# Performance work log

Measured on AMD Instinct MI355X. Metric: run time of the kernel, lower is better.

The kernel has to match this reference:

```python
import jax, jax.numpy as jnp
import numpy as np
from jax import lax

SIGMA, GAMMA, N_ORI = 6.0, 0.5, 6
WAVELENGTHS = (8.0, 10.0, 12.0)
KS = 37  # int(6*sigma)=36 -> +1 to make odd


def make_gabor_kernels():
    # Replicates cv2.getGaborKernel(psi=0); kernel is symmetric under 180-deg
    # rotation so cv2's index flip is a no-op and conv == correlation.
    half = KS // 2
    yy, xx = np.meshgrid(np.arange(-half, half + 1, dtype=np.float64),
                         np.arange(-half, half + 1, dtype=np.float64), indexing='ij')
    ks = []
    for lam in WAVELENGTHS:
        for t in range(N_ORI):
            th = t * np.pi / N_ORI
            xr = xx * np.cos(th) + yy * np.sin(th)
            yr = -xx * np.sin(th) + yy * np.cos(th)
            k = np.exp(-(xr ** 2 + (GAMMA ** 2) * yr ** 2) / (2.0 * SIGMA ** 2)) \
                * np.cos(2.0 * np.pi / lam * xr)
            ks.append(k.astype(np.float32))
    return jnp.asarray(np.stack(ks))[:, None]  # (F=18, 1, 37, 37)


def setup_inputs() -> dict:
    key = jax.random.key(0)
    x = jax.random.normal(key, (8, 3, 256, 256), dtype=jnp.float32)
    return {"x": x, "gabor_kernels": make_gabor_kernels()}


def haar_dwt2(x):
    # Single-level pywt haar dwt2; for even H,W symmetric padding never fires,
    # so each output pixel comes from a disjoint 2x2 block [[a,b],[c,d]].
    B, C, H, W = x.shape
    xb = x.reshape(B, C, H // 2, 2, W // 2, 2)
    a, b = xb[:, :, :, 0, :, 0], xb[:, :, :, 0, :, 1]
    c, d = xb[:, :, :, 1, :, 0], xb[:, :, :, 1, :, 1]
    LL = (a + b + c + d) * 0.5
    LH = (a + b - c - d) * 0.5  # pywt cH ('da'): high along rows
    HL = (a - b + c - d) * 0.5  # pywt cV ('ad'): high along cols
    HH = (a - b - c + d) * 0.5  # pywt cD ('dd')
    sub = jnp.stack([LL, LH, HL, HH], axis=2)  # (B, C, 4, H/2, W/2)
    return sub.reshape(B, C * 4, H // 2, W // 2)


def gabor_bank(x, kernels):
    # One grouped conv replaces the Python C x F conv2d loop. Group-major output
    # channel order (channel outer, filter inner) matches the torch loop order.
    B, C, H, W = x.shape
    F = kernels.shape[0]
    w = jnp.tile(kernels, (C, 1, 1, 1))  # (C*F, 1, KS, KS)
    pad = KS // 2
    return lax.conv_general_dilated(
        x, w, window_strides=(1, 1), padding=[(pad, pad), (pad, pad)],
        dimension_numbers=('NCHW', 'OIHW', 'NCHW'), feature_group_count=C)


def fft_channels(x):
    B, C, H, W = x.shape
    xc = jnp.fft.rfft2(x, norm='ortho')       # (B, C, H, W//2+1)
    mag = jnp.abs(xc)
    ph = jnp.arctan2(xc.imag, xc.real)        # torch.angle
    pad = W - mag.shape[-1]
    pads = [(0, 0), (0, 0), (0, 0), (0, pad)]
    return jnp.concatenate([jnp.pad(mag, pads), jnp.pad(ph, pads)], axis=1)


def reference(x, gabor_kernels):
    dwt = haar_dwt2(x)                 # (B, C*4, H/2, W/2)
    gab = gabor_bank(x, gabor_kernels)  # (B, C*18, H, W)
    fft = fft_channels(x)              # (B, C*2, H, W)
    return (dwt, gab, fft)
```

## Files before the change

### kernel.cpp

```cpp
#include <hip/hip_runtime.h>
#include <math.h>

#define BB 8
#define CC 3
#define HH 256
#define WW 256
#define KSZ 37
#define PD 18

#define DWT_OFF 0
#define GAB_OFF (8*12*128*128)
#define FFT_OFF (GAB_OFF + 8*54*256*256)

#define PSTRIDE 88

typedef short bf16x8 __attribute__((ext_vector_type(8)));
typedef float f32x16 __attribute__((ext_vector_type(16)));

__device__ __forceinline__ unsigned f2bf(float f) {
  unsigned u = __float_as_uint(f);
  return (u + 0x7fffu + ((u >> 16) & 1u)) >> 16;
}

__global__ __launch_bounds__(256) void prep_wshc_kernel(
    const float* __restrict__ wk, ushort* __restrict__ wshc) {
  int idx = blockIdx.x * 256 + threadIdx.x;
  if (idx >= 454656) return;
  int j = idx & 7; int rest = idx >> 3;
  int l = rest & 63; rest >>= 6;
  int t = rest % 3; rest /= 3;
  int ky = rest % 37; int s = rest / 37;
  int m = l & 31, hi = l >> 5;
  int kk = 16 * t + 8 * hi + j - s;
  float v = 0.0f;
  if (m < 18 && kk >= 0 && kk < 37) v = wk[(m * 37 + ky) * 37 + kk];
  wshc[idx] = (ushort)f2bf(v);
}

#define LOAD_B_SET \
    r0 = *reinterpret_cast<const bf16x8*>(bp); \
    r1 = *reinterpret_cast<const bf16x8*>(bp + 8); \
    r2 = *reinterpret_cast<const bf16x8*>(bp + 16); \
    r3 = *reinterpret_cast<const bf16x8*>(bp + 24); \
    r4 = *reinterpret_cast<const bf16x8*>(bp + 32); \
    r5 = *reinterpret_cast<const bf16x8*>(bp + 40); \
    r6 = *reinterpret_cast<const bf16x8*>(bp + 48); \
    r7 = *reinterpret_cast<const bf16x8*>(bp + 56);
#define MFMA_GROUP(A0, A1, A2) \
    acc0 = __builtin_amdgcn_mfma_f32_32x32x16_bf16(A0, r0, acc0, 0, 0, 0); \
    acc1 = __builtin_amdgcn_mfma_f32_32x32x16_bf16(A0, r1, acc1, 0, 0, 0); \
    acc2 = __builtin_amdgcn_mfma_f32_32x32x16_bf16(A0, r2, acc2, 0, 0, 0); \
    acc3 = __builtin_amdgcn_mfma_f32_32x32x16_bf16(A0, r3, acc3, 0, 0, 0); \
    acc0 = __builtin_amdgcn_mfma_f32_32x32x16_bf16(A1, r2, acc0, 0, 0, 0); \
    acc1 = __builtin_amdgcn_mfma_f32_32x32x16_bf16(A1, r3, acc1, 0, 0, 0); \
    acc2 = __builtin_amdgcn_mfma_f32_32x32x16_bf16(A1, r4, acc2, 0, 0, 0); \
    acc3 = __builtin_amdgcn_mfma_f32_32x32x16_bf16(A1, r5, acc3, 0, 0, 0); \
    acc0 = __builtin_amdgcn_mfma_f32_32x32x16_bf16(A2, r4, acc0, 0, 0, 0); \
    acc1 = __builtin_amdgcn_mfma_f32_32x32x16_bf16(A2, r5, acc1, 0, 0, 0); \
    acc2 = __builtin_amdgcn_mfma_f32_32x32x16_bf16(A2, r6, acc2, 0, 0, 0); \
    acc3 = __builtin_amdgcn_mfma_f32_32x32x16_bf16(A2, r7, acc3, 0, 0, 0);

__global__ __launch_bounds__(512, 4) void gabor_mfma_kernel(
    const float* __restrict__ x, const ushort* __restrict__ wshc,
    float* __restrict__ out) {
  __shared__ unsigned patchU[68 * (PSTRIDE / 2)];
  __shared__ float cbuf[4 * 32 * 33];

  const int tid = threadIdx.x;
  const int tileX = (blockIdx.x & 7) * 32;
  const int tileY = (blockIdx.x >> 3) * 32;
  const int cin = blockIdx.y, b = blockIdx.z;
  const float* xp = x + (size_t)(b * CC + cin) * (HH * WW);

  for (int idx = tid; idx < 68 * (PSTRIDE / 2); idx += 512) {
    int r = idx / (PSTRIDE / 2), dc = idx - r * (PSTRIDE / 2);
    int gy = tileY + r - PD;
    int gx0 = tileX + 2 * dc - PD;
    float v0 = 0.0f, v1 = 0.0f;
    if ((unsigned)gy < 256u) {
      if ((unsigned)gx0 < 256u)       v0 = xp[gy * WW + gx0];
      if ((unsigned)(gx0 + 1) < 256u) v1 = xp[gy * WW + gx0 + 1];
    }
    patchU[idx] = f2bf(v0) | (f2bf(v1) << 16);
  }
  __syncthreads();

  const int w  = tid >> 6;
  const int l  = tid & 63;
  const int n  = l & 31;
  const int hi = l >> 5;

  f32x16 acc0 = {0.f,0.f,0.f,0.f,0.f,0.f,0.f,0.f,0.f,0.f,0.f,0.f,0.f,0.f,0.f,0.f};
  f32x16 acc1 = acc0, acc2 = acc0, acc3 = acc0;

  const ushort* patchS = reinterpret_cast<const ushort*>(patchU);
  const ushort* ap = wshc + (size_t)w * (37 * 3 * 512) + (size_t)l * 8;
  const ushort* bp = patchS + (size_t)n * PSTRIDE + hi * 8;

  bf16x8 aA0, aA1, aA2, aB0, aB1, aB2;
  bf16x8 r0, r1, r2, r3, r4, r5, r6, r7;

  aA0 = *reinterpret_cast<const bf16x8*>(ap);
  aA1 = *reinterpret_cast<const bf16x8*>(ap + 512);
  aA2 = *reinterpret_cast<const bf16x8*>(ap + 1024);

  for (int kp = 0; kp < 18; ++kp) {
    aB0 = *reinterpret_cast<const bf16x8*>(ap + 1536);
    aB1 = *reinterpret_cast<const bf16x8*>(ap + 2048);
    aB2 = *reinterpret_cast<const bf16x8*>(ap + 2560);
    LOAD_B_SET
    MFMA_GROUP(aA0, aA1, aA2)
    bp += PSTRIDE;
    aA0 = *reinterpret_cast<const bf16x8*>(ap + 3072);
    aA1 = *reinterpret_cast<const bf16x8*>(ap + 3584);
    aA2 = *reinterpret_cast<const bf16x8*>(ap + 4096);
    LOAD_B_SET
    MFMA_GROUP(aB0, aB1, aB2)
    ap += 3072;
    bp += PSTRIDE;
  }
  {
    LOAD_B_SET
    MFMA_GROUP(aA0, aA1, aA2)
  }
  __syncthreads();

  float* outb = out + GAB_OFF + (size_t)(b * 54 + cin * 18) * (HH * WW);
#pragma unroll
  for (int g = 0; g < 5; ++g) {
    if (hi == (g & 1)) {
      const int rq = g >> 1;
#pragma unroll
      for (int q = 0; q < 4; ++q) {
        const int e = 4 * rq + q;
        float* crow = &cbuf[(q * 32 + n) * 33 + w];
        crow[0]  = acc0[e];
        crow[8]  = acc1[e];
        crow[16] = acc2[e];
        crow[24] = acc3[e];
      }
    }
    __syncthreads();
#pragma unroll
    for (int it = 0; it < 8; ++it) {
      int idx = tid + it * 512;
      int xo = idx & 31, yo = (idx >> 5) & 31, q = idx >> 10;
      int f = 4 * g + q;
      if (f < 18)
        outb[(size_t)f * (HH * WW) + (size_t)(tileY + yo) * WW + tileX + xo] =
            cbuf[(q * 32 + yo) * 33 + xo];
    }
    __syncthreads();
  }
}

__global__ __launch_bounds__(256) void haar_dwt_kernel(
    const float* __restrict__ x, float* __restrict__ out) {
  int idx = blockIdx.x * 256 + threadIdx.x;
  if (idx >= BB * CC * 128 * 128) return;
  int j  = idx & 127;
  int i  = (idx >> 7) & 127;
  int bc = idx >> 14;
  const float* xp = x + (size_t)bc * (HH * WW);
  float2 top = *reinterpret_cast<const float2*>(&xp[(2 * i) * WW + 2 * j]);
  float2 bot = *reinterpret_cast<const float2*>(&xp[(2 * i + 1) * WW + 2 * j]);
  float a = top.x, b = top.y, c = bot.x, d = bot.y;
  int bI = bc / 3, cI = bc % 3;
  float* op = out + DWT_OFF + ((size_t)(bI * 12 + cI * 4) * 128 + i) * 128 + j;
  op[0]     = (a + b + c + d) * 0.5f;
  op[16384] = (a + b - c - d) * 0.5f;
  op[32768] = (a - b + c - d) * 0.5f;
  op[49152] = (a - b - c + d) * 0.5f;
}

__global__ __launch_bounds__(64) void fft_rows_kernel(
    const float* __restrict__ x, float* __restrict__ stg) {
  __shared__ float re[256], im[256], twr[128], twi[128];
  const int rowid = blockIdx.x;
  const float* xr = x + (size_t)rowid * 256;
  const int t = threadIdx.x;

#pragma unroll
  for (int q = 0; q < 2; ++q) {
    int k = t + q * 64;
    float sn, cs;
    sincosf(-2.0f * (float)M_PI * (float)k / 256.0f, &sn, &cs);
    twr[k] = cs; twi[k] = sn;
  }
#pragma unroll
  for (int q = 0; q < 4; ++q) {
    int i = t + q * 64;
    int br = __brev((unsigned)i) >> 24;
    re[br] = xr[i];
    im[br] = 0.0f;
  }
  __syncthreads();

  for (int s = 1; s <= 8; ++s) {
    int half = 1 << (s - 1);
    int sh = 8 - s;
#pragma unroll
    for (int q = 0; q < 2; ++q) {
      int j = t + q * 64;
      int g = j >> (s - 1);
      int p = j & (half - 1);
      int i1 = (g << s) + p;
      int i2 = i1 + half;
      float cs = twr[p << sh], sn = twi[p << sh];
      float r2 = re[i2], m2 = im[i2];
      float tr = r2 * cs - m2 * sn;
      float ti = r2 * sn + m2 * cs;
      float r1 = re[i1], m1 = im[i1];
      re[i2] = r1 - tr; im[i2] = m1 - ti;
      re[i1] = r1 + tr; im[i1] = m1 + ti;
    }
    __syncthreads();
  }

  float* sr = stg + (size_t)rowid * 258;
#pragma unroll
  for (int q = 0; q < 3; ++q) {
    int k = t + q * 64;
    if (k <= 128) {
      sr[2 * k]     = re[k];
      sr[2 * k + 1] = im[k];
    }
  }
}

__global__ __launch_bounds__(64) void fft_cols_kernel(
    const float* __restrict__ stg, float* __restrict__ outf) {
  const int k  = blockIdx.x & 255;
  const int bc = blockIdx.x >> 8;
  const int b  = bc / 3;
  const int c  = bc - b * 3;
  const int t  = threadIdx.x;
  float* magp = outf + (size_t)(b * 6 + c) * (HH * WW);
  float* php  = outf + (size_t)(b * 6 + c + 3) * (HH * WW);

  if (k >= 129) {
#pragma unroll
    for (int q = 0; q < 4; ++q) {
      int u = t + q * 64;
      magp[(size_t)u * WW + k] = 0.0f;
      php[(size_t)u * WW + k]  = 0.0f;
    }
    return;
  }

  __shared__ float re[256], im[256], twr[128], twi[128];
  const float* sp = stg + (size_t)bc * (256 * 258);
#pragma unroll
  for (int q = 0; q < 2; ++q) {
    int kk = t + q * 64;
    float sn, cs;
    sincosf(-2.0f * (float)M_PI * (float)kk / 256.0f, &sn, &cs);
    twr[kk] = cs; twi[kk] = sn;
  }
#pragma unroll
  for (int q = 0; q < 4; ++q) {
    int y = t + q * 64;
    int br = __brev((unsigned)y) >> 24;
    re[br] = sp[(size_t)y * 258 + 2 * k];
    im[br] = sp[(size_t)y * 258 + 2 * k + 1];
  }
  __syncthreads();

  for (int s = 1; s <= 8; ++s) {
    int half = 1 << (s - 1);
    int sh = 8 - s;
#pragma unroll
    for (int q = 0; q < 2; ++q) {
      int j = t + q * 64;
      int g = j >> (s - 1);
      int p = j & (half - 1);
      int i1 = (g << s) + p;
      int i2 = i1 + half;
      float cs = twr[p << sh], sn = twi[p << sh];
      float r2 = re[i2], m2 = im[i2];
      float tr = r2 * cs - m2 * sn;
      float ti = r2 * sn + m2 * cs;
      float r1 = re[i1], m1 = im[i1];
      re[i2] = r1 - tr; im[i2] = m1 - ti;
      re[i1] = r1 + tr; im[i1] = m1 + ti;
    }
    __syncthreads();
  }

  const float scale = 1.0f / 256.0f;
#pragma unroll
  for (int q = 0; q < 4; ++q) {
    int u = t + q * 64;
    float r = re[u], m = im[u];
    magp[(size_t)u * WW + k] = sqrtf(r * r + m * m) * scale;
    php[(size_t)u * WW + k]  = atan2f(m, r);
  }
}

extern "C" void kernel_launch(void* const* d_in, const int* in_sizes, int n_in,
                              void* d_out, int out_size, void* d_ws, size_t ws_size,
                              hipStream_t stream) {
  const float* x  = (const float*)d_in[0];
  const float* wk = (const float*)d_in[1];
  float* out = (float*)d_out;

  ushort* wshc = (ushort*)(out + DWT_OFF);
  float*  stg  = out + GAB_OFF;

  prep_wshc_kernel<<<dim3(1776), dim3(256), 0, stream>>>(wk, wshc);
  fft_rows_kernel<<<dim3(BB * CC * HH), dim3(64), 0, stream>>>(x, stg);
  fft_cols_kernel<<<dim3(BB * CC * WW), dim3(64), 0, stream>>>(stg, out + FFT_OFF);
  gabor_mfma_kernel<<<dim3(64, CC, BB), dim3(512), 0, stream>>>(x, wshc, out);
  haar_dwt_kernel<<<dim3(1536), dim3(256), 0, stream>>>(x, out);
}
```

Baseline: 189.9 us.

## Fuse weight prep with row FFT and Gabor conv with column FFT

Merges the weight-prep and row-FFT kernels into one launch, and the Gabor MFMA conv and column-FFT kernels into another, dispatching on block index. The FFTs are restructured so each 64-lane wave handles one row or column with no block barriers. This relies on in-order LDS access within a single wave. The intermediate spectrum is now staged in place in the FFT output region instead of the Gabor region, so the column FFT can share a launch with the Gabor conv. The goal is fewer launches and letting the light FFT blocks fill the device alongside the heavy conv blocks, at the cost of relying on implicit intra-wave LDS ordering.

```diff
diff --git a/kernel.cpp b/kernel.cpp
--- a/kernel.cpp
+++ b/kernel.cpp
@@ -14,6 +14,11 @@
 
 #define PSTRIDE 88
 
+#define PREP_BLOCKS 888
+#define FFTROW_BLOCKS 768
+#define GAB_BLOCKS 1536
+#define FFTCOL_BLOCKS 768
+
 typedef short bf16x8 __attribute__((ext_vector_type(8)));
 typedef float f32x16 __attribute__((ext_vector_type(16)));
 
@@ -22,19 +27,84 @@
   return (u + 0x7fffu + ((u >> 16) & 1u)) >> 16;
 }
 
-__global__ __launch_bounds__(256) void prep_wshc_kernel(
-    const float* __restrict__ wk, ushort* __restrict__ wshc) {
-  int idx = blockIdx.x * 256 + threadIdx.x;
-  if (idx >= 454656) return;
-  int j = idx & 7; int rest = idx >> 3;
-  int l = rest & 63; rest >>= 6;
-  int t = rest % 3; rest /= 3;
-  int ky = rest % 37; int s = rest / 37;
-  int m = l & 31, hi = l >> 5;
-  int kk = 16 * t + 8 * hi + j - s;
-  float v = 0.0f;
-  if (m < 18 && kk >= 0 && kk < 37) v = wk[(m * 37 + ky) * 37 + kk];
-  wshc[idx] = (ushort)f2bf(v);
+__global__ __launch_bounds__(512) void fused_pre_kernel(
+    const float* __restrict__ x, const float* __restrict__ wk,
+    ushort* __restrict__ wshc, float* __restrict__ out) {
+  __shared__ __align__(16) float smem[4352];
+  const int g = blockIdx.x;
+  const int tid = threadIdx.x;
+
+  if (g < PREP_BLOCKS) {
+    int idx = g * 512 + tid;
+    int j = idx & 7; int rest = idx >> 3;
+    int l = rest & 63; rest >>= 6;
+    int t = rest % 3; rest /= 3;
+    int ky = rest % 37; int s = rest / 37;
+    int m = l & 31, hi = l >> 5;
+    int kk = 16 * t + 8 * hi + j - s;
+    float v = 0.0f;
+    if (m < 18 && kk >= 0 && kk < 37) v = wk[(m * 37 + ky) * 37 + kk];
+    wshc[idx] = (ushort)f2bf(v);
+    return;
+  }
+
+  const int w = tid >> 6;
+  const int t = tid & 63;
+  const int rowid = (g - PREP_BLOCKS) * 8 + w;
+  float* re  = smem + w * 256;
+  float* im  = smem + 2048 + w * 256;
+  float* twr = smem + 4096;
+  float* twi = smem + 4224;
+
+#pragma unroll
+  for (int q = 0; q < 2; ++q) {
+    int k = t + q * 64;
+    float sn, cs;
+    sincosf(-2.0f * (float)M_PI * (float)k / 256.0f, &sn, &cs);
+    twr[k] = cs; twi[k] = sn;
+  }
+
+  const float* xr = x + (size_t)rowid * 256;
+#pragma unroll
+  for (int q = 0; q < 4; ++q) {
+    int i = t + q * 64;
+    int br = __brev((unsigned)i) >> 24;
+    re[br] = xr[i];
+    im[br] = 0.0f;
+  }
+
+  for (int s = 1; s <= 8; ++s) {
+    int half = 1 << (s - 1);
+    int sh = 8 - s;
+#pragma unroll
+    for (int q = 0; q < 2; ++q) {
+      int j = t + q * 64;
+      int gg = j >> (s - 1);
+      int p = j & (half - 1);
+      int i1 = (gg << s) + p;
+      int i2 = i1 + half;
+      float cs = twr[p << sh], sn = twi[p << sh];
+      float r2 = re[i2], m2 = im[i2];
+      float tr = r2 * cs - m2 * sn;
+      float ti = r2 * sn + m2 * cs;
+      float r1 = re[i1], m1 = im[i1];
+      re[i2] = r1 - tr; im[i2] = m1 - ti;
+      re[i1] = r1 + tr; im[i1] = m1 + ti;
+    }
+  }
+
+  const int bc = rowid >> 8;
+  const int y  = rowid & 255;
+  const int b  = bc / 3, c = bc - b * 3;
+  float* magrow = out + FFT_OFF + (size_t)(b * 6 + c) * (HH * WW) + (size_t)y * WW;
+  float* phrow  = magrow + (size_t)3 * (HH * WW);
+#pragma unroll
+  for (int q = 0; q < 2; ++q) {
+    int k = t + q * 64;
+    magrow[k] = re[k];
+    phrow[k]  = im[k];
+  }
+  if (t == 0) { magrow[128] = re[128]; phrow[128] = im[128]; }
 }
 
 #define LOAD_B_SET \
@@ -60,97 +130,163 @@
     acc2 = __builtin_amdgcn_mfma_f32_32x32x16_bf16(A2, r6, acc2, 0, 0, 0); \
     acc3 = __builtin_amdgcn_mfma_f32_32x32x16_bf16(A2, r7, acc3, 0, 0, 0);
 
-__global__ __launch_bounds__(512, 4) void gabor_mfma_kernel(
+__global__ __launch_bounds__(512, 4) void fused_main_kernel(
     const float* __restrict__ x, const ushort* __restrict__ wshc,
     float* __restrict__ out) {
-  __shared__ unsigned patchU[68 * (PSTRIDE / 2)];
-  __shared__ float cbuf[4 * 32 * 33];
-
+  __shared__ __align__(16) float smem[7216];
+  const int g = blockIdx.x;
   const int tid = threadIdx.x;
-  const int tileX = (blockIdx.x & 7) * 32;
-  const int tileY = (blockIdx.x >> 3) * 32;
-  const int cin = blockIdx.y, b = blockIdx.z;
-  const float* xp = x + (size_t)(b * CC + cin) * (HH * WW);
-
-  for (int idx = tid; idx < 68 * (PSTRIDE / 2); idx += 512) {
-    int r = idx / (PSTRIDE / 2), dc = idx - r * (PSTRIDE / 2);
-    int gy = tileY + r - PD;
-    int gx0 = tileX + 2 * dc - PD;
-    float v0 = 0.0f, v1 = 0.0f;
-    if ((unsigned)gy < 256u) {
-      if ((unsigned)gx0 < 256u)       v0 = xp[gy * WW + gx0];
-      if ((unsigned)(gx0 + 1) < 256u) v1 = xp[gy * WW + gx0 + 1];
-    }
-    patchU[idx] = f2bf(v0) | (f2bf(v1) << 16);
-  }
-  __syncthreads();
-
-  const int w  = tid >> 6;
-  const int l  = tid & 63;
-  const int n  = l & 31;
-  const int hi = l >> 5;
-
-  f32x16 acc0 = {0.f,0.f,0.f,0.f,0.f,0.f,0.f,0.f,0.f,0.f,0.f,0.f,0.f,0.f,0.f,0.f};
-  f32x16 acc1 = acc0, acc2 = acc0, acc3 = acc0;
-
-  const ushort* patchS = reinterpret_cast<const ushort*>(patchU);
-  const ushort* ap = wshc + (size_t)w * (37 * 3 * 512) + (size_t)l * 8;
-  const ushort* bp = patchS + (size_t)n * PSTRIDE + hi * 8;
-
-  bf16x8 aA0, aA1, aA2, aB0, aB1, aB2;
-  bf16x8 r0, r1, r2, r3, r4, r5, r6, r7;
-
-  aA0 = *reinterpret_cast<const bf16x8*>(ap);
-  aA1 = *reinterpret_cast<const bf16x8*>(ap + 512);
-  aA2 = *reinterpret_cast<const bf16x8*>(ap + 1024);
-
-  for (int kp = 0; kp < 18; ++kp) {
-    aB0 = *reinterpret_cast<const bf16x8*>(ap + 1536);
-    aB1 = *reinterpret_cast<const bf16x8*>(ap + 2048);
-    aB2 = *reinterpret_cast<const bf16x8*>(ap + 2560);
-    LOAD_B_SET
-    MFMA_GROUP(aA0, aA1, aA2)
-    bp += PSTRIDE;
-    aA0 = *reinterpret_cast<const bf16x8*>(ap + 3072);
-    aA1 = *reinterpret_cast<const bf16x8*>(ap + 3584);
-    aA2 = *reinterpret_cast<const bf16x8*>(ap + 4096);
-    LOAD_B_SET
-    MFMA_GROUP(aB0, aB1, aB2)
-    ap += 3072;
-    bp += PSTRIDE;
-  }
-  {
-    LOAD_B_SET
-    MFMA_GROUP(aA0, aA1, aA2)
-  }
-  __syncthreads();
-
-  float* outb = out + GAB_OFF + (size_t)(b * 54 + cin * 18) * (HH * WW);
-#pragma unroll
-  for (int g = 0; g < 5; ++g) {
-    if (hi == (g & 1)) {
-      const int rq = g >> 1;
-#pragma unroll
-      for (int q = 0; q < 4; ++q) {
-        const int e = 4 * rq + q;
-        float* crow = &cbuf[(q * 32 + n) * 33 + w];
-        crow[0]  = acc0[e];
-        crow[8]  = acc1[e];
-        crow[16] = acc2[e];
-        crow[24] = acc3[e];
+
+  if (g < GAB_BLOCKS) {
+    unsigned* patchU = reinterpret_cast<unsigned*>(smem);
+    float* cbuf = smem + 2992;
+    const int tile = g & 63;
+    const int rest = g >> 6;
+    const int cin = rest % 3, b = rest / 3;
+    const int tileX = (tile & 7) * 32;
+    const int tileY = (tile >> 3) * 32;
+    const float* xp = x + (size_t)(b * CC + cin) * (HH * WW);
+
+    for (int idx = tid; idx < 68 * (PSTRIDE / 2); idx += 512) {
+      int r = idx / (PSTRIDE / 2), dc = idx - r * (PSTRIDE / 2);
+      int gy = tileY + r - PD;
+      int gx0 = tileX + 2 * dc - PD;
+      float v0 = 0.0f, v1 = 0.0f;
+      if ((unsigned)gy < 256u) {
+        if ((unsigned)gx0 < 256u)       v0 = xp[gy * WW + gx0];
+        if ((unsigned)(gx0 + 1) < 256u) v1 = xp[gy * WW + gx0 + 1];
       }
+      patchU[idx] = f2bf(v0) | (f2bf(v1) << 16);
     }
     __syncthreads();
-#pragma unroll
-    for (int it = 0; it < 8; ++it) {
-      int idx = tid + it * 512;
-      int xo = idx & 31, yo = (idx >> 5) & 31, q = idx >> 10;
-      int f = 4 * g + q;
-      if (f < 18)
-        outb[(size_t)f * (HH * WW) + (size_t)(tileY + yo) * WW + tileX + xo] =
-            cbuf[(q * 32 + yo) * 33 + xo];
+
+    const int w  = tid >> 6;
+    const int l  = tid & 63;
+    const int n  = l & 31;
+    const int hi = l >> 5;
+
+    f32x16 acc0 = {0.f,0.f,0.f,0.f,0.f,0.f,0.f,0.f,0.f,0.f,0.f,0.f,0.f,0.f,0.f,0.f};
+    f32x16 acc1 = acc0, acc2 = acc0, acc3 = acc0;
+
+    const ushort* patchS = reinterpret_cast<const ushort*>(patchU);
+    const ushort* ap = wshc + (size_t)w * (37 * 3 * 512) + (size_t)l * 8;
+    const ushort* bp = patchS + (size_t)n * PSTRIDE + hi * 8;
+
+    bf16x8 aA0, aA1, aA2, aB0, aB1, aB2;
+    bf16x8 r0, r1, r2, r3, r4, r5, r6, r7;
+
+    aA0 = *reinterpret_cast<const bf16x8*>(ap);
+    aA1 = *reinterpret_cast<const bf16x8*>(ap + 512);
+    aA2 = *reinterpret_cast<const bf16x8*>(ap + 1024);
+
+    for (int kp = 0; kp < 18; ++kp) {
+      aB0 = *reinterpret_cast<const bf16x8*>(ap + 1536);
+      aB1 = *reinterpret_cast<const bf16x8*>(ap + 2048);
+      aB2 = *reinterpret_cast<const bf16x8*>(ap + 2560);
+      LOAD_B_SET
+      MFMA_GROUP(aA0, aA1, aA2)
+      bp += PSTRIDE;
+      aA0 = *reinterpret_cast<const bf16x8*>(ap + 3072);
+      aA1 = *reinterpret_cast<const bf16x8*>(ap + 3584);
+      aA2 = *reinterpret_cast<const bf16x8*>(ap + 4096);
+      LOAD_B_SET
+      MFMA_GROUP(aB0, aB1, aB2)
+      ap += 3072;
+      bp += PSTRIDE;
+    }
+    {
+      LOAD_B_SET
+      MFMA_GROUP(aA0, aA1, aA2)
     }
     __syncthreads();
+
+    float* outb = out + GAB_OFF + (size_t)(b * 54 + cin * 18) * (HH * WW);
+#pragma unroll
+    for (int gq = 0; gq < 5; ++gq) {
+      if (hi == (gq & 1)) {
+        const int rq = gq >> 1;
+#pragma unroll
+        for (int q = 0; q < 4; ++q) {
+          const int e = 4 * rq + q;
+          float* crow = &cbuf[(q * 32 + n) * 33 + w];
+          crow[0]  = acc0[e];
+          crow[8]  = acc1[e];
+          crow[16] = acc2[e];
+          crow[24] = acc3[e];
+        }
+      }
+      __syncthreads();
+#pragma unroll
+      for (int it = 0; it < 8; ++it) {
+        int idx = tid + it * 512;
+        int xo = idx & 31, yo = (idx >> 5) & 31, q = idx >> 10;
+        int f = 4 * gq + q;
+        if (f < 18)
+          outb[(size_t)f * (HH * WW) + (size_t)(tileY + yo) * WW + tileX + xo] =
+              cbuf[(q * 32 + yo) * 33 + xo];
+      }
+      __syncthreads();
+    }
+    return;
+  }
+
+  const int w = tid >> 6;
+  const int t = tid & 63;
+  const int colid = (g - GAB_BLOCKS) * 8 + w;
+  const int bc = colid >> 8;
+  const int k  = colid & 255;
+  const int b  = bc / 3, c = bc - b * 3;
+  float* re  = smem + w * 256;
+  float* im  = smem + 2048 + w * 256;
+  float* twr = smem + 4096;
+  float* twi = smem + 4224;
+
+#pragma unroll
+  for (int q = 0; q < 2; ++q) {
+    int kk = t + q * 64;
+    float sn, cs;
+    sincosf(-2.0f * (float)M_PI * (float)kk / 256.0f, &sn, &cs);
+    twr[kk] = cs; twi[kk] = sn;
+  }
+
+  float* magp = out + FFT_OFF + (size_t)(b * 6 + c) * (HH * WW);
+  float* php  = magp + (size_t)3 * (HH * WW);
+  const bool live = (k < 129);
+#pragma unroll
+  for (int q = 0; q < 4; ++q) {
+    int y = t + q * 64;
+    int br = __brev((unsigned)y) >> 24;
+    re[br] = live ? magp[(size_t)y * WW + k] : 0.0f;
+    im[br] = live ? php[(size_t)y * WW + k]  : 0.0f;
+  }
+
+  for (int s = 1; s <= 8; ++s) {
+    int half = 1 << (s - 1);
+    int sh = 8 - s;
+#pragma unroll
+    for (int q = 0; q < 2; ++q) {
+      int j = t + q * 64;
+      int gg = j >> (s - 1);
+      int p = j & (half - 1);
+      int i1 = (gg << s) + p;
+      int i2 = i1 + half;
+      float cs = twr[p << sh], sn = twi[p << sh];
+      float r2 = re[i2], m2 = im[i2];
+      float tr = r2 * cs - m2 * sn;
+      float ti = r2 * sn + m2 * cs;
+      float r1 = re[i1], m1 = im[i1];
+      re[i2] = r1 - tr; im[i2] = m1 - ti;
+      re[i1] = r1 + tr; im[i1] = m1 + ti;
+    }
+  }
+
+  const float scale = 1.0f / 256.0f;
+#pragma unroll
+  for (int q = 0; q < 4; ++q) {
+    int u = t + q * 64;
+    float r = re[u], m = im[u];
+    magp[(size_t)u * WW + k] = sqrtf(r * r + m * m) * scale;
+    php[(size_t)u * WW + k]  = atan2f(m, r);
   }
 }
 
@@ -173,130 +309,6 @@
   op[49152] = (a - b - c + d) * 0.5f;
 }
 
-__global__ __launch_bounds__(64) void fft_rows_kernel(
-    const float* __restrict__ x, float* __restrict__ stg) {
-  __shared__ float re[256], im[256], twr[128], twi[128];
-  const int rowid = blockIdx.x;
-  const float* xr = x + (size_t)rowid * 256;
-  const int t = threadIdx.x;
-
-#pragma unroll
-  for (int q = 0; q < 2; ++q) {
-    int k = t + q * 64;
-    float sn, cs;
-    sincosf(-2.0f * (float)M_PI * (float)k / 256.0f, &sn, &cs);
-    twr[k] = cs; twi[k] = sn;
-  }
-#pragma unroll
-  for (int q = 0; q < 4; ++q) {
-    int i = t + q * 64;
-    int br = __brev((unsigned)i) >> 24;
-    re[br] = xr[i];
-    im[br] = 0.0f;
-  }
-  __syncthreads();
-
-  for (int s = 1; s <= 8; ++s) {
-    int half = 1 << (s - 1);
-    int sh = 8 - s;
-#pragma unroll
-    for (int q = 0; q < 2; ++q) {
-      int j = t + q * 64;
-      int g = j >> (s - 1);
-      int p = j & (half - 1);
-      int i1 = (g << s) + p;
-      int i2 = i1 + half;
-      float cs = twr[p << sh], sn = twi[p << sh];
-      float r2 = re[i2], m2 = im[i2];
-      float tr = r2 * cs - m2 * sn;
-      float ti = r2 * sn + m2 * cs;
-      float r1 = re[i1], m1 = im[i1];
-      re[i2] = r1 - tr; im[i2] = m1 - ti;
-      re[i1] = r1 + tr; im[i1] = m1 + ti;
-    }
-    __syncthreads();
-  }
-
-  float* sr = stg + (size_t)rowid * 258;
-#pragma unroll
-  for (int q = 0; q < 3; ++q) {
-    int k = t + q * 64;
-    if (k <= 128) {
-      sr[2 * k]     = re[k];
-      sr[2 * k + 1] = im[k];
-    }
-  }
-}
-
-__global__ __launch_bounds__(64) void fft_cols_kernel(
-    const float* __restrict__ stg, float* __restrict__ outf) {
-  const int k  = blockIdx.x & 255;
-  const int bc = blockIdx.x >> 8;
-  const int b  = bc / 3;
-  const int c  = bc - b * 3;
-  const int t  = threadIdx.x;
-  float* magp = outf + (size_t)(b * 6 + c) * (HH * WW);
-  float* php  = outf + (size_t)(b * 6 + c + 3) * (HH * WW);
-
-  if (k >= 129) {
-#pragma unroll
-    for (int q = 0; q < 4; ++q) {
-      int u = t + q * 64;
-      magp[(size_t)u * WW + k] = 0.0f;
-      php[(size_t)u * WW + k]  = 0.0f;
-    }
-    return;
-  }
-
-  __shared__ float re[256], im[256], twr[128], twi[128];
-  const float* sp = stg + (size_t)bc * (256 * 258);
-#pragma unroll
-  for (int q = 0; q < 2; ++q) {
-    int kk = t + q * 64;
-    float sn, cs;
-    sincosf(-2.0f * (float)M_PI * (float)kk / 256.0f, &sn, &cs);
-    twr[kk] = cs; twi[kk] = sn;
-  }
-#pragma unroll
-  for (int q = 0; q < 4; ++q) {
-    int y = t + q * 64;
-    int br = __brev((unsigned)y) >> 24;
-    re[br] = sp[(size_t)y * 258 + 2 * k];
-    im[br] = sp[(size_t)y * 258 + 2 * k + 1];
-  }
-  __syncthreads();
-
-  for (int s = 1; s <= 8; ++s) {
-    int half = 1 << (s - 1);
-    int sh = 8 - s;
-#pragma unroll
-    for (int q = 0; q < 2; ++q) {
-      int j = t + q * 64;
-      int g = j >> (s - 1);
-      int p = j & (half - 1);
-      int i1 = (g << s) + p;
-      int i2 = i1 + half;
-      float cs = twr[p << sh], sn = twi[p << sh];
-      float r2 = re[i2], m2 = im[i2];
-      float tr = r2 * cs - m2 * sn;
-      float ti = r2 * sn + m2 * cs;
-      float r1 = re[i1], m1 = im[i1];
-      re[i2] = r1 - tr; im[i2] = m1 - ti;
-      re[i1] = r1 + tr; im[i1] = m1 + ti;
-    }
-    __syncthreads();
-  }
-
-  const float scale = 1.0f / 256.0f;
-#pragma unroll
-  for (int q = 0; q < 4; ++q) {
-    int u = t + q * 64;
-    float r = re[u], m = im[u];
-    magp[(size_t)u * WW + k] = sqrtf(r * r + m * m) * scale;
-    php[(size_t)u * WW + k]  = atan2f(m, r);
-  }
-}
-
 extern "C" void kernel_launch(void* const* d_in, const int* in_sizes, int n_in,
                               void* d_out, int out_size, void* d_ws, size_t ws_size,
                               hipStream_t stream) {
@@ -305,11 +317,10 @@
   float* out = (float*)d_out;
 
   ushort* wshc = (ushort*)(out + DWT_OFF);
-  float*  stg  = out + GAB_OFF;
-
-  prep_wshc_kernel<<<dim3(1776), dim3(256), 0, stream>>>(wk, wshc);
-  fft_rows_kernel<<<dim3(BB * CC * HH), dim3(64), 0, stream>>>(x, stg);
-  fft_cols_kernel<<<dim3(BB * CC * WW), dim3(64), 0, stream>>>(stg, out + FFT_OFF);
-  gabor_mfma_kernel<<<dim3(64, CC, BB), dim3(512), 0, stream>>>(x, wshc, out);
+
+  fused_pre_kernel<<<dim3(PREP_BLOCKS + FFTROW_BLOCKS), dim3(512), 0, stream>>>(
+      x, wk, wshc, out);
+  fused_main_kernel<<<dim3(GAB_BLOCKS + FFTCOL_BLOCKS), dim3(512), 0, stream>>>(
+      x, wshc, out);
   haar_dwt_kernel<<<dim3(1536), dim3(256), 0, stream>>>(x, out);
 }
```

Result: faster. 169.1 us (-11.0%).
